# Performance work log

Hardware: AMD Instinct MI355X
Metric: run time of the kernel (lower is better)

## Reference

```python
import jax, jax.numpy as jnp
import numpy as np

NUM_HEADS = 16
EPS = 1e-6
MAX_POS = 1000

def _pos_encoding(position, d):
    pos = np.arange(position)[:, None].astype(np.float32)
    i = np.arange(d)[None, :].astype(np.float32)
    angle = pos / np.power(10000.0, 2.0 * np.floor(i / 2.0) / np.float32(d))
    angle[:, 0::2] = np.sin(angle[:, 0::2])
    angle[:, 1::2] = np.cos(angle[:, 1::2])
    return jnp.asarray(angle[None], dtype=jnp.float32)  # [1, position, d]

def _layernorm(x, g, b):
    m = x.mean(-1, keepdims=True)
    v = ((x - m) ** 2).mean(-1, keepdims=True)
    return (x - m) * jax.lax.rsqrt(v + EPS) * g + b

def setup_inputs() -> dict:
    key = jax.random.key(0)
    L, D, F, B, S = 6, 1024, 4096, 4, 512
    sd = 0.02
    ks = jax.random.split(key, 8)
    return {
        "x": jax.random.normal(ks[0], (B, S, D), jnp.float32),
        "mask": jnp.zeros((B, 1, 1, S), jnp.float32),
        "Wq": sd * jax.random.normal(ks[1], (L, D, D), jnp.float32),
        "bq": jnp.zeros((L, D), jnp.float32),
        "Wk": sd * jax.random.normal(ks[2], (L, D, D), jnp.float32),
        "bk": jnp.zeros((L, D), jnp.float32),
        "Wv": sd * jax.random.normal(ks[3], (L, D, D), jnp.float32),
        "bv": jnp.zeros((L, D), jnp.float32),
        "Wo": sd * jax.random.normal(ks[4], (L, D, D), jnp.float32),
        "bo": jnp.zeros((L, D), jnp.float32),
        "W1": sd * jax.random.normal(ks[5], (L, D, F), jnp.float32),
        "b1": jnp.zeros((L, F), jnp.float32),
        "W2": sd * jax.random.normal(ks[6], (L, F, D), jnp.float32),
        "b2": jnp.zeros((L, D), jnp.float32),
        "g1": jnp.ones((L, D), jnp.float32),
        "be1": jnp.zeros((L, D), jnp.float32),
        "g2": jnp.ones((L, D), jnp.float32),
        "be2": jnp.zeros((L, D), jnp.float32),
    }

def reference(x, mask, Wq, bq, Wk, bk, Wv, bv, Wo, bo, W1, b1, W2, b2, g1, be1, g2, be2):
    B, S, D = x.shape
    H = NUM_HEADS
    depth = D // H
    scale = 1.0 / jnp.sqrt(jnp.float32(depth))
    x = x + _pos_encoding(MAX_POS, D)[:, :S, :]

    def layer(h, p):
        (wq, bq_, wk, bk_, wv, bv_, wo, bo_, w1, b1_, w2, b2_, g1_, be1_, g2_, be2_) = p
        split = lambda t: t.reshape(B, S, H, depth).transpose(0, 2, 1, 3)
        q = split(h @ wq + bq_)
        k = split(h @ wk + bk_)
        v = split(h @ wv + bv_)
        logits = jnp.einsum('bhqd,bhkd->bhqk', q, k) * scale + mask * (-1e9)
        a = jax.nn.softmax(logits, axis=-1)
        o = jnp.einsum('bhqk,bhkd->bhqd', a, v).transpose(0, 2, 1, 3).reshape(B, S, D)
        o = o @ wo + bo_
        h1 = _layernorm(h + o, g1_, be1_)
        f = jax.nn.relu(h1 @ w1 + b1_) @ w2 + b2_
        return _layernorm(h1 + f, g2_, be2_), None

    out, _ = jax.lax.scan(layer, x, (Wq, bq, Wk, bk, Wv, bv, Wo, bo, W1, b1, W2, b2, g1, be1, g2, be2))
    return out
```

## Files before the change

kernel.cpp:

```cpp
#include <hip/hip_runtime.h>

typedef __attribute__((ext_vector_type(8))) short bf16x8;
typedef __attribute__((ext_vector_type(4))) float f32x4;
typedef unsigned short u16;

#define D_MODEL 1024
#define SEQ 512
#define BATCH 4
#define NH 16
#define FF 4096
#define NLAYER 6
#define NTOKS 2048

__device__ __forceinline__ u16 f2bf(float f) {
  unsigned int u = __float_as_uint(f);
  u += 0x7fffu + ((u >> 16) & 1u);
  return (u16)(u >> 16);
}

__device__ __forceinline__ void gload16(const void* g, void* lds) {
  __builtin_amdgcn_global_load_lds((const __attribute__((address_space(1))) void*)g,
                                   (__attribute__((address_space(3))) void*)lds, 16, 0, 0);
}

__global__ __launch_bounds__(256) void posenc_k(const float* __restrict__ x, float* __restrict__ h,
                                                u16* __restrict__ hb) {
  int row = blockIdx.x;
  int s = row & (SEQ - 1);
  int t = threadIdx.x;
  float4 v = *(const float4*)(x + (size_t)row * D_MODEL + t * 4);
  float r[4] = {v.x, v.y, v.z, v.w};
#pragma unroll
  for (int j = 0; j < 4; ++j) {
    int d = t * 4 + j;
    int p = d >> 1;
    float ang = (float)s * exp2f((float)p * (-2.0f / 1024.0f) * 13.287712379549449f);
    r[j] += (d & 1) ? cosf(ang) : sinf(ang);
  }
  float4 o = {r[0], r[1], r[2], r[3]};
  *(float4*)(h + (size_t)row * D_MODEL + t * 4) = o;
  ushort4 ob;
  ob.x = f2bf(r[0]); ob.y = f2bf(r[1]); ob.z = f2bf(r[2]); ob.w = f2bf(r[3]);
  *(ushort4*)(hb + (size_t)row * D_MODEL + t * 4) = ob;
}

#define WTP 72
__device__ __forceinline__ void wconv_body(const float* __restrict__ src, u16* __restrict__ dst,
                                           int K, int N, float scale, int nb, int kb) {
  __shared__ u16 tile[64 * WTP];
  const int t = threadIdx.x;
#pragma unroll
  for (int rr = 0; rr < 4; ++rr) {
    int k = (t >> 4) + rr * 16;
    int n4 = (t & 15) * 4;
    float4 v = *(const float4*)(src + (size_t)(kb + k) * N + nb + n4);
    tile[(n4 + 0) * WTP + k] = f2bf(v.x * scale);
    tile[(n4 + 1) * WTP + k] = f2bf(v.y * scale);
    tile[(n4 + 2) * WTP + k] = f2bf(v.z * scale);
    tile[(n4 + 3) * WTP + k] = f2bf(v.w * scale);
  }
  __syncthreads();
#pragma unroll
  for (int rr = 0; rr < 2; ++rr) {
    int n = (t >> 3) + rr * 32;
    int kq = (t & 7) * 8;
    uint4 v = *(const uint4*)&tile[n * WTP + kq];
    *(uint4*)&dst[(size_t)(nb + n) * K + kb + kq] = v;
  }
}

__global__ __launch_bounds__(256) void wconv_qkv_k(const float* __restrict__ Wq,
                                                   const float* __restrict__ Wk,
                                                   const float* __restrict__ Wv,
                                                   u16* __restrict__ dst) {
  int z = blockIdx.z, l = z / 3, which = z % 3;
  const float* src = (which == 0 ? Wq : which == 1 ? Wk : Wv) + (size_t)l * 1024 * 1024;
  u16* d = dst + (size_t)l * 3072 * 1024 + (size_t)which * 1024 * 1024;
  float scale = (which == 0) ? 0.125f : 1.0f;
  wconv_body(src, d, 1024, 1024, scale, blockIdx.x * 64, blockIdx.y * 64);
}

__global__ __launch_bounds__(256) void wconv_gen_k(const float* __restrict__ W, u16* __restrict__ dst,
                                                   int K, int N) {
  int z = blockIdx.z;
  wconv_body(W + (size_t)z * K * N, dst + (size_t)z * N * K, K, N, 1.0f,
             blockIdx.x * 64, blockIdx.y * 64);
}

__global__ __launch_bounds__(256) void bqkv_k(const float* bq, const float* bk, const float* bv,
                                              float* o) {
  int i = blockIdx.x * 256 + threadIdx.x;
  int l = i / 3072, j = i % 3072;
  float v = (j < 1024) ? bq[l * 1024 + j] * 0.125f
                       : (j < 2048 ? bk[l * 1024 + j - 1024] : bv[l * 1024 + j - 2048]);
  o[i] = v;
}

template <int OBF, int RELU, int KSPLIT>
__global__ __launch_bounds__(256) void gemm64_k(const u16* __restrict__ A, const u16* __restrict__ Bt,
                                                const float* __restrict__ bias, void* __restrict__ Cv,
                                                int N, int K) {
  __shared__ u16 As[4][64 * 32];
  __shared__ u16 Bs[4][64 * 32];
  const int t = threadIdx.x, lane = t & 63, wave = t >> 6;
  const int wm = wave >> 1, wn = wave & 1;
  const int lrow = lane & 15, lgrp = lane >> 4;
  const int m0 = blockIdx.y * 64, n0 = blockIdx.x * 64;
  const int kseg = K / KSPLIT;
  const int koff = (KSPLIT > 1) ? blockIdx.z * kseg : 0;

  f32x4 acc[2][2];
#pragma unroll
  for (int i = 0; i < 2; ++i)
#pragma unroll
    for (int j = 0; j < 2; ++j) acc[i][j] = (f32x4){0.f, 0.f, 0.f, 0.f};

  const u16* Ag = A + (size_t)m0 * K + koff;
  const u16* Bg = Bt + (size_t)n0 * K + koff;
  const int ebase = wave * 512;
  const int e = ebase + lane * 8;
  const int srow = e >> 5, skc = e & 31;

  auto stage = [&](int buf, int k0) {
    gload16(Ag + (size_t)srow * K + k0 + skc, &As[buf][ebase]);
    gload16(Bg + (size_t)srow * K + k0 + skc, &Bs[buf][ebase]);
  };

  const int nk = kseg / 32;
  stage(0, 0);
  stage(1, 32);
  stage(2, 64);
  for (int tt = 0; tt < nk; ++tt) {
    if (tt + 2 < nk) asm volatile("s_waitcnt vmcnt(4)" ::: "memory");
    else if (tt + 1 < nk) asm volatile("s_waitcnt vmcnt(2)" ::: "memory");
    else asm volatile("s_waitcnt vmcnt(0)" ::: "memory");
    __builtin_amdgcn_s_barrier();
    __builtin_amdgcn_sched_barrier(0);
    if (tt + 3 < nk) stage((tt + 3) & 3, (tt + 3) * 32);
    const int cur = tt & 3;
    bf16x8 af[2], bfr[2];
#pragma unroll
    for (int i = 0; i < 2; ++i)
      af[i] = *(const bf16x8*)&As[cur][(wm * 32 + i * 16 + lrow) * 32 + lgrp * 8];
#pragma unroll
    for (int j = 0; j < 2; ++j)
      bfr[j] = *(const bf16x8*)&Bs[cur][(wn * 32 + j * 16 + lrow) * 32 + lgrp * 8];
#pragma unroll
    for (int i = 0; i < 2; ++i)
#pragma unroll
      for (int j = 0; j < 2; ++j)
        acc[i][j] = __builtin_amdgcn_mfma_f32_16x16x32_bf16(af[i], bfr[j], acc[i][j], 0, 0, 0);
  }

  const size_t outoff = (KSPLIT > 1) ? (size_t)blockIdx.z * NTOKS * N : 0;
#pragma unroll
  for (int j = 0; j < 2; ++j) {
    int col = n0 + wn * 32 + j * 16 + lrow;
    float bv = (KSPLIT == 1 || blockIdx.z == 0) ? bias[col] : 0.f;
#pragma unroll
    for (int i = 0; i < 2; ++i) {
      int rowb = m0 + wm * 32 + i * 16 + lgrp * 4;
#pragma unroll
      for (int r = 0; r < 4; ++r) {
        float v = acc[i][j][r] + bv;
        if (RELU) v = fmaxf(v, 0.f);
        if (OBF)
          ((u16*)Cv)[(size_t)(rowb + r) * N + col] = f2bf(v);
        else
          ((float*)Cv)[outoff + (size_t)(rowb + r) * N + col] = v;
      }
    }
  }
}

__global__ __launch_bounds__(256) void vtrans_k(const u16* __restrict__ qkv, u16* __restrict__ vt) {
  __shared__ u16 tile[32][33];
  const int bx = blockIdx.x, by = blockIdx.y, b = blockIdx.z;
  const int tx = threadIdx.x & 31, ty = threadIdx.x >> 5;
#pragma unroll
  for (int i = 0; i < 32; i += 8) {
    int sidx = bx * 32 + ty + i, d = by * 32 + tx;
    tile[ty + i][tx] = qkv[(size_t)(b * SEQ + sidx) * 3072 + 2048 + d];
  }
  __syncthreads();
#pragma unroll
  for (int i = 0; i < 32; i += 8) {
    int d = by * 32 + ty + i, sidx = bx * 32 + tx;
    vt[(size_t)(b * D_MODEL + d) * SEQ + sidx] = tile[tx][ty + i];
  }
}

#define KPAD 72
__global__ __launch_bounds__(256) void attn_k(const u16* __restrict__ qkv, const u16* __restrict__ vt,
                                              const float* __restrict__ mask, u16* __restrict__ o) {
  __shared__ u16 Ks[64 * KPAD];
  __shared__ u16 Vs[64 * KPAD];
  __shared__ u16 Ps[64 * KPAD];
  const int t = threadIdx.x;
  const int lane = t & 63, wave = t >> 6;
  const int lrow = lane & 15, lgrp = lane >> 4;
  const int qb = blockIdx.x;
  const int bh = blockIdx.y;
  const int b = bh >> 4, hh = bh & 15;

  bf16x8 qf[2];
  const int qrow0 = qb * 64 + wave * 16;
#pragma unroll
  for (int kk = 0; kk < 2; ++kk)
    qf[kk] = *(const bf16x8*)(qkv + (size_t)(b * SEQ + qrow0 + lrow) * 3072 +
                              hh * 64 + kk * 32 + lgrp * 8);

  float mreg[4], lsum[4];
  f32x4 oacc[4];
#pragma unroll
  for (int r = 0; r < 4; ++r) { mreg[r] = -1e30f; lsum[r] = 0.f; }
#pragma unroll
  for (int dn = 0; dn < 4; ++dn) oacc[dn] = (f32x4){0.f, 0.f, 0.f, 0.f};

  const int sr = t >> 3, sc = t & 7;
  for (int it = 0; it < 8; ++it) {
    const int kv0 = it * 64;
#pragma unroll
    for (int half = 0; half < 2; ++half) {
      int r = sr + half * 32;
      uint4 kv4 = *(const uint4*)(qkv + (size_t)(b * SEQ + kv0 + r) * 3072 + 1024 + hh * 64 + sc * 8);
      *(uint4*)(&Ks[r * KPAD + sc * 8]) = kv4;
      uint4 vv4 = *(const uint4*)(vt + (size_t)(bh * 64 + r) * SEQ + kv0 + sc * 8);
      *(uint4*)(&Vs[r * KPAD + sc * 8]) = vv4;
    }
    __syncthreads();

    f32x4 s[4];
#pragma unroll
    for (int nt = 0; nt < 4; ++nt) s[nt] = (f32x4){0.f, 0.f, 0.f, 0.f};
#pragma unroll
    for (int nt = 0; nt < 4; ++nt)
#pragma unroll
      for (int kk = 0; kk < 2; ++kk) {
        bf16x8 kf = *(const bf16x8*)(&Ks[(nt * 16 + lrow) * KPAD + kk * 32 + lgrp * 8]);
        s[nt] = __builtin_amdgcn_mfma_f32_16x16x32_bf16(qf[kk], kf, s[nt], 0, 0, 0);
      }
    float mv[4];
#pragma unroll
    for (int nt = 0; nt < 4; ++nt) mv[nt] = mask[b * SEQ + kv0 + nt * 16 + lrow] * -1e9f;
#pragma unroll
    for (int nt = 0; nt < 4; ++nt)
#pragma unroll
      for (int r = 0; r < 4; ++r) s[nt][r] = s[nt][r] + mv[nt];

#pragma unroll
    for (int r = 0; r < 4; ++r) {
      float mx = fmaxf(fmaxf(s[0][r], s[1][r]), fmaxf(s[2][r], s[3][r]));
      mx = fmaxf(mx, __shfl_xor(mx, 1));
      mx = fmaxf(mx, __shfl_xor(mx, 2));
      mx = fmaxf(mx, __shfl_xor(mx, 4));
      mx = fmaxf(mx, __shfl_xor(mx, 8));
      float mnew = fmaxf(mreg[r], mx);
      float corr = __expf(mreg[r] - mnew);
      mreg[r] = mnew;
      float p0 = __expf(s[0][r] - mnew);
      float p1 = __expf(s[1][r] - mnew);
      float p2 = __expf(s[2][r] - mnew);
      float p3 = __expf(s[3][r] - mnew);
      float rs = p0 + p1 + p2 + p3;
      rs += __shfl_xor(rs, 1);
      rs += __shfl_xor(rs, 2);
      rs += __shfl_xor(rs, 4);
      rs += __shfl_xor(rs, 8);
      lsum[r] = lsum[r] * corr + rs;
#pragma unroll
      for (int dn = 0; dn < 4; ++dn) oacc[dn][r] = oacc[dn][r] * corr;
      int prow = wave * 16 + lgrp * 4 + r;
      Ps[prow * KPAD + 0 + lrow] = f2bf(p0);
      Ps[prow * KPAD + 16 + lrow] = f2bf(p1);
      Ps[prow * KPAD + 32 + lrow] = f2bf(p2);
      Ps[prow * KPAD + 48 + lrow] = f2bf(p3);
    }
    __syncthreads();
#pragma unroll
    for (int kk = 0; kk < 2; ++kk) {
      bf16x8 pf = *(const bf16x8*)(&Ps[(wave * 16 + lrow) * KPAD + kk * 32 + lgrp * 8]);
#pragma unroll
      for (int dn = 0; dn < 4; ++dn) {
        bf16x8 vf = *(const bf16x8*)(&Vs[(dn * 16 + lrow) * KPAD + kk * 32 + lgrp * 8]);
        oacc[dn] = __builtin_amdgcn_mfma_f32_16x16x32_bf16(pf, vf, oacc[dn], 0, 0, 0);
      }
    }
    __syncthreads();
  }
#pragma unroll
  for (int dn = 0; dn < 4; ++dn)
#pragma unroll
    for (int r = 0; r < 4; ++r) {
      int qrow = qrow0 + lgrp * 4 + r;
      o[(size_t)(b * SEQ + qrow) * D_MODEL + hh * 64 + dn * 16 + lrow] =
          f2bf(oacc[dn][r] / lsum[r]);
    }
}

__global__ __launch_bounds__(256) void ln_k(const float* __restrict__ res, const float* __restrict__ p0,
                                            const float* __restrict__ p1, const float* __restrict__ g,
                                            const float* __restrict__ be, float* __restrict__ out,
                                            u16* __restrict__ outb) {
  __shared__ float red[8];
  const int row = blockIdx.x, t = threadIdx.x;
  float4 va = *(const float4*)(res + (size_t)row * D_MODEL + t * 4);
  float4 vb = *(const float4*)(p0 + (size_t)row * D_MODEL + t * 4);
  float4 vc = *(const float4*)(p1 + (size_t)row * D_MODEL + t * 4);
  float x0 = va.x + vb.x + vc.x, x1 = va.y + vb.y + vc.y;
  float x2 = va.z + vb.z + vc.z, x3 = va.w + vb.w + vc.w;
  float s = x0 + x1 + x2 + x3;
  float s2 = x0 * x0 + x1 * x1 + x2 * x2 + x3 * x3;
#pragma unroll
  for (int off = 1; off < 64; off <<= 1) {
    s += __shfl_xor(s, off);
    s2 += __shfl_xor(s2, off);
  }
  const int wave = t >> 6, lane = t & 63;
  if (lane == 0) { red[wave] = s; red[4 + wave] = s2; }
  __syncthreads();
  s = red[0] + red[1] + red[2] + red[3];
  s2 = red[4] + red[5] + red[6] + red[7];
  float mean = s * (1.f / D_MODEL);
  float var = s2 * (1.f / D_MODEL) - mean * mean;
  float inv = rsqrtf(var + 1e-6f);
  float4 vg = *(const float4*)(g + t * 4);
  float4 ve = *(const float4*)(be + t * 4);
  float4 r;
  r.x = (x0 - mean) * inv * vg.x + ve.x;
  r.y = (x1 - mean) * inv * vg.y + ve.y;
  r.z = (x2 - mean) * inv * vg.z + ve.z;
  r.w = (x3 - mean) * inv * vg.w + ve.w;
  *(float4*)(out + (size_t)row * D_MODEL + t * 4) = r;
  if (outb) {
    ushort4 w;
    w.x = f2bf(r.x); w.y = f2bf(r.y); w.z = f2bf(r.z); w.w = f2bf(r.w);
    *(ushort4*)(outb + (size_t)row * D_MODEL + t * 4) = w;
  }
}

extern "C" void kernel_launch(void* const* d_in, const int* in_sizes, int n_in,
                              void* d_out, int out_size, void* d_ws, size_t ws_size,
                              hipStream_t stream) {
  const float* x = (const float*)d_in[0];
  const float* mask = (const float*)d_in[1];
  const float* Wq = (const float*)d_in[2];
  const float* bq = (const float*)d_in[3];
  const float* Wk = (const float*)d_in[4];
  const float* bk = (const float*)d_in[5];
  const float* Wv = (const float*)d_in[6];
  const float* bv = (const float*)d_in[7];
  const float* Wo = (const float*)d_in[8];
  const float* bo = (const float*)d_in[9];
  const float* W1 = (const float*)d_in[10];
  const float* b1 = (const float*)d_in[11];
  const float* W2 = (const float*)d_in[12];
  const float* b2 = (const float*)d_in[13];
  const float* g1 = (const float*)d_in[14];
  const float* be1 = (const float*)d_in[15];
  const float* g2 = (const float*)d_in[16];
  const float* be2 = (const float*)d_in[17];
  float* out = (float*)d_out;

  const size_t NTOK = (size_t)BATCH * SEQ;
  const size_t ACT = NTOK * D_MODEL;
  char* w = (char*)d_ws;
  float* h = (float*)w;     w += ACT * 4;
  float* h1 = (float*)w;    w += ACT * 4;
  float* op = (float*)w;    w += ACT * 4 * 2;
  u16* hb = (u16*)w;        w += ACT * 2;
  u16* h1b = (u16*)w;       w += ACT * 2;
  u16* qkvb = (u16*)w;      w += NTOK * 3072 * 2;
  u16* vt_ = (u16*)w;       w += ACT * 2;
  u16* obb = (u16*)w;       w += ACT * 2;
  u16* tb = (u16*)w;        w += NTOK * FF * 2;
  u16* wqkv_all = (u16*)w;  w += (size_t)NLAYER * 3072 * 1024 * 2;
  u16* wo_all = (u16*)w;    w += (size_t)NLAYER * 1024 * 1024 * 2;
  u16* w1_all = (u16*)w;    w += (size_t)NLAYER * 4096 * 1024 * 2;
  u16* w2_all = (u16*)w;    w += (size_t)NLAYER * 1024 * 4096 * 2;
  float* bqkv_all = (float*)w; w += (size_t)NLAYER * 3072 * 4;

  posenc_k<<<(int)NTOK, 256, 0, stream>>>(x, h, hb);
  wconv_qkv_k<<<dim3(16, 16, 18), 256, 0, stream>>>(Wq, Wk, Wv, wqkv_all);
  wconv_gen_k<<<dim3(16, 16, 6), 256, 0, stream>>>(Wo, wo_all, 1024, 1024);
  wconv_gen_k<<<dim3(64, 16, 6), 256, 0, stream>>>(W1, w1_all, 1024, 4096);
  wconv_gen_k<<<dim3(16, 64, 6), 256, 0, stream>>>(W2, w2_all, 4096, 1024);
  bqkv_k<<<72, 256, 0, stream>>>(bq, bk, bv, bqkv_all);

  for (int l = 0; l < NLAYER; ++l) {
    const u16* wqkv_t = wqkv_all + (size_t)l * 3072 * 1024;
    const u16* wo_t = wo_all + (size_t)l * 1024 * 1024;
    const u16* w1_t = w1_all + (size_t)l * 4096 * 1024;
    const u16* w2_t = w2_all + (size_t)l * 1024 * 4096;
    const float* bqkvl = bqkv_all + (size_t)l * 3072;
    const float* bol = bo + (size_t)l * D_MODEL;
    const float* b1l = b1 + (size_t)l * FF;
    const float* b2l = b2 + (size_t)l * D_MODEL;
    const float* g1l = g1 + (size_t)l * D_MODEL;
    const float* be1l = be1 + (size_t)l * D_MODEL;
    const float* g2l = g2 + (size_t)l * D_MODEL;
    const float* be2l = be2 + (size_t)l * D_MODEL;

    gemm64_k<1, 0, 1><<<dim3(48, 32), 256, 0, stream>>>(hb, wqkv_t, bqkvl, qkvb, 3072, 1024);
    vtrans_k<<<dim3(16, 32, 4), 256, 0, stream>>>(qkvb, vt_);
    attn_k<<<dim3(8, 64), 256, 0, stream>>>(qkvb, vt_, mask, obb);
    gemm64_k<0, 0, 2><<<dim3(16, 32, 2), 256, 0, stream>>>(obb, wo_t, bol, op, 1024, 1024);
    ln_k<<<(int)NTOK, 256, 0, stream>>>(h, op, op + ACT, g1l, be1l, h1, h1b);
    gemm64_k<1, 1, 1><<<dim3(64, 32), 256, 0, stream>>>(h1b, w1_t, b1l, tb, 4096, 1024);
    gemm64_k<0, 0, 2><<<dim3(16, 32, 2), 256, 0, stream>>>(tb, w2_t, b2l, op, 1024, 4096);
    ln_k<<<(int)NTOK, 256, 0, stream>>>(h1, op, op + ACT, g2l, be2l, (l == NLAYER - 1) ? out : h, hb);
  }
}
```

Measured before the change: 1.163 ms.

## Enlarge GEMM tiles to 128x128 with LDS swizzle, XCD remap and split-K 4

Replaces the 64x64 GEMM with a 128x128 tile per block. Each wave now computes a 64x64 sub-tile of 16 MFMAs per k-step, which cuts global and LDS traffic per flop. It adds an XOR swizzle on LDS columns to avoid bank conflicts, a workgroup remap so neighbouring tiles land on the same XCD, and s_setprio around MFMA bursts in the GEMM and attention kernels. Split-K for the Wo and W2 GEMMs goes from 2 to 4 to keep enough blocks, so the layernorm now sums 4 partial buffers, which adds extra fp32 traffic.

```diff
diff --git a/kernel.cpp b/kernel.cpp
--- a/kernel.cpp
+++ b/kernel.cpp
@@ -97,33 +97,49 @@
 }
 
 template <int OBF, int RELU, int KSPLIT>
-__global__ __launch_bounds__(256) void gemm64_k(const u16* __restrict__ A, const u16* __restrict__ Bt,
-                                                const float* __restrict__ bias, void* __restrict__ Cv,
-                                                int N, int K) {
-  __shared__ u16 As[4][64 * 32];
-  __shared__ u16 Bs[4][64 * 32];
+__global__ __launch_bounds__(256) void gemm128_k(const u16* __restrict__ A, const u16* __restrict__ Bt,
+                                                 const float* __restrict__ bias, void* __restrict__ Cv,
+                                                 int N, int K) {
+  __shared__ u16 As[4][128 * 32];
+  __shared__ u16 Bs[4][128 * 32];
   const int t = threadIdx.x, lane = t & 63, wave = t >> 6;
   const int wm = wave >> 1, wn = wave & 1;
   const int lrow = lane & 15, lgrp = lane >> 4;
-  const int m0 = blockIdx.y * 64, n0 = blockIdx.x * 64;
+
+  const int GX = N >> 7;
+  const int nwg = GX * 16;
+  int flat = blockIdx.y * GX + blockIdx.x;
+  int q = nwg >> 3, r = nwg & 7, xcd = flat & 7, pos = flat >> 3;
+  int logical = (xcd < r ? xcd * (q + 1) : r * (q + 1) + (xcd - r) * q) + pos;
+  const int m0 = (logical & 15) * 128, n0 = (logical >> 4) * 128;
+
   const int kseg = K / KSPLIT;
   const int koff = (KSPLIT > 1) ? blockIdx.z * kseg : 0;
 
-  f32x4 acc[2][2];
-#pragma unroll
-  for (int i = 0; i < 2; ++i)
-#pragma unroll
-    for (int j = 0; j < 2; ++j) acc[i][j] = (f32x4){0.f, 0.f, 0.f, 0.f};
+  f32x4 acc[4][4];
+#pragma unroll
+  for (int i = 0; i < 4; ++i)
+#pragma unroll
+    for (int j = 0; j < 4; ++j) acc[i][j] = (f32x4){0.f, 0.f, 0.f, 0.f};
 
   const u16* Ag = A + (size_t)m0 * K + koff;
   const u16* Bg = Bt + (size_t)n0 * K + koff;
-  const int ebase = wave * 512;
-  const int e = ebase + lane * 8;
-  const int srow = e >> 5, skc = e & 31;
 
   auto stage = [&](int buf, int k0) {
-    gload16(Ag + (size_t)srow * K + k0 + skc, &As[buf][ebase]);
-    gload16(Bg + (size_t)srow * K + k0 + skc, &Bs[buf][ebase]);
+#pragma unroll
+    for (int rr = 0; rr < 2; ++rr) {
+      int s = rr * 256 + t;
+      int row = s >> 2, cst = s & 3;
+      int csrc = cst ^ ((row >> 1) & 3);
+      gload16(Ag + (size_t)row * K + k0 + csrc * 8, &As[buf][s * 8]);
+    }
+#pragma unroll
+    for (int rr = 0; rr < 2; ++rr) {
+      int s = rr * 256 + t;
+      int row = s >> 2, cst = s & 3;
+      int csrc = cst ^ ((row >> 1) & 3);
+      gload16(Bg + (size_t)row * K + k0 + csrc * 8, &Bs[buf][s * 8]);
+    }
   };
 
   const int nk = kseg / 32;
@@ -131,35 +147,43 @@
   stage(1, 32);
   stage(2, 64);
   for (int tt = 0; tt < nk; ++tt) {
-    if (tt + 2 < nk) asm volatile("s_waitcnt vmcnt(4)" ::: "memory");
-    else if (tt + 1 < nk) asm volatile("s_waitcnt vmcnt(2)" ::: "memory");
+    if (tt + 2 < nk) asm volatile("s_waitcnt vmcnt(8)" ::: "memory");
+    else if (tt + 1 < nk) asm volatile("s_waitcnt vmcnt(4)" ::: "memory");
     else asm volatile("s_waitcnt vmcnt(0)" ::: "memory");
     __builtin_amdgcn_s_barrier();
     __builtin_amdgcn_sched_barrier(0);
     if (tt + 3 < nk) stage((tt + 3) & 3, (tt + 3) * 32);
     const int cur = tt & 3;
-    bf16x8 af[2], bfr[2];
-#pragma unroll
-    for (int i = 0; i < 2; ++i)
-      af[i] = *(const bf16x8*)&As[cur][(wm * 32 + i * 16 + lrow) * 32 + lgrp * 8];
-#pragma unroll
-    for (int j = 0; j < 2; ++j)
-      bfr[j] = *(const bf16x8*)&Bs[cur][(wn * 32 + j * 16 + lrow) * 32 + lgrp * 8];
-#pragma unroll
-    for (int i = 0; i < 2; ++i)
-#pragma unroll
-      for (int j = 0; j < 2; ++j)
+    bf16x8 af[4], bfr[4];
+#pragma unroll
+    for (int i = 0; i < 4; ++i) {
+      int row = wm * 64 + i * 16 + lrow;
+      int sl = lgrp ^ ((row >> 1) & 3);
+      af[i] = *(const bf16x8*)&As[cur][row * 32 + sl * 8];
+    }
+#pragma unroll
+    for (int j = 0; j < 4; ++j) {
+      int row = wn * 64 + j * 16 + lrow;
+      int sl = lgrp ^ ((row >> 1) & 3);
+      bfr[j] = *(const bf16x8*)&Bs[cur][row * 32 + sl * 8];
+    }
+    __builtin_amdgcn_s_setprio(1);
+#pragma unroll
+    for (int i = 0; i < 4; ++i)
+#pragma unroll
+      for (int j = 0; j < 4; ++j)
         acc[i][j] = __builtin_amdgcn_mfma_f32_16x16x32_bf16(af[i], bfr[j], acc[i][j], 0, 0, 0);
+    __builtin_amdgcn_s_setprio(0);
   }
 
   const size_t outoff = (KSPLIT > 1) ? (size_t)blockIdx.z * NTOKS * N : 0;
 #pragma unroll
-  for (int j = 0; j < 2; ++j) {
-    int col = n0 + wn * 32 + j * 16 + lrow;
+  for (int j = 0; j < 4; ++j) {
+    int col = n0 + wn * 64 + j * 16 + lrow;
     float bv = (KSPLIT == 1 || blockIdx.z == 0) ? bias[col] : 0.f;
 #pragma unroll
-    for (int i = 0; i < 2; ++i) {
-      int rowb = m0 + wm * 32 + i * 16 + lgrp * 4;
+    for (int i = 0; i < 4; ++i) {
+      int rowb = m0 + wm * 64 + i * 16 + lgrp * 4;
 #pragma unroll
       for (int r = 0; r < 4; ++r) {
         float v = acc[i][j][r] + bv;
@@ -233,6 +257,7 @@
     f32x4 s[4];
 #pragma unroll
     for (int nt = 0; nt < 4; ++nt) s[nt] = (f32x4){0.f, 0.f, 0.f, 0.f};
+    __builtin_amdgcn_s_setprio(1);
 #pragma unroll
     for (int nt = 0; nt < 4; ++nt)
 #pragma unroll
@@ -240,6 +265,7 @@
         bf16x8 kf = *(const bf16x8*)(&Ks[(nt * 16 + lrow) * KPAD + kk * 32 + lgrp * 8]);
         s[nt] = __builtin_amdgcn_mfma_f32_16x16x32_bf16(qf[kk], kf, s[nt], 0, 0, 0);
       }
+    __builtin_amdgcn_s_setprio(0);
     float mv[4];
 #pragma unroll
     for (int nt = 0; nt < 4; ++nt) mv[nt] = mask[b * SEQ + kv0 + nt * 16 + lrow] * -1e9f;
@@ -277,6 +303,7 @@
       Ps[prow * KPAD + 48 + lrow] = f2bf(p3);
     }
     __syncthreads();
+    __builtin_amdgcn_s_setprio(1);
 #pragma unroll
     for (int kk = 0; kk < 2; ++kk) {
       bf16x8 pf = *(const bf16x8*)(&Ps[(wave * 16 + lrow) * KPAD + kk * 32 + lgrp * 8]);
@@ -286,6 +313,7 @@
         oacc[dn] = __builtin_amdgcn_mfma_f32_16x16x32_bf16(pf, vf, oacc[dn], 0, 0, 0);
       }
     }
+    __builtin_amdgcn_s_setprio(0);
     __syncthreads();
   }
 #pragma unroll
@@ -298,17 +326,19 @@
     }
 }
 
-__global__ __launch_bounds__(256) void ln_k(const float* __restrict__ res, const float* __restrict__ p0,
-                                            const float* __restrict__ p1, const float* __restrict__ g,
-                                            const float* __restrict__ be, float* __restrict__ out,
-                                            u16* __restrict__ outb) {
+template <int P>
+__global__ __launch_bounds__(256) void ln_k(const float* __restrict__ res, const float* __restrict__ parts,
+                                            const float* __restrict__ g, const float* __restrict__ be,
+                                            float* __restrict__ out, u16* __restrict__ outb) {
   __shared__ float red[8];
   const int row = blockIdx.x, t = threadIdx.x;
   float4 va = *(const float4*)(res + (size_t)row * D_MODEL + t * 4);
-  float4 vb = *(const float4*)(p0 + (size_t)row * D_MODEL + t * 4);
-  float4 vc = *(const float4*)(p1 + (size_t)row * D_MODEL + t * 4);
-  float x0 = va.x + vb.x + vc.x, x1 = va.y + vb.y + vc.y;
-  float x2 = va.z + vb.z + vc.z, x3 = va.w + vb.w + vc.w;
+  float x0 = va.x, x1 = va.y, x2 = va.z, x3 = va.w;
+#pragma unroll
+  for (int p = 0; p < P; ++p) {
+    float4 vp = *(const float4*)(parts + (size_t)p * NTOKS * D_MODEL + (size_t)row * D_MODEL + t * 4);
+    x0 += vp.x; x1 += vp.y; x2 += vp.z; x3 += vp.w;
+  }
   float s = x0 + x1 + x2 + x3;
   float s2 = x0 * x0 + x1 * x1 + x2 * x2 + x3 * x3;
 #pragma unroll
@@ -367,7 +397,7 @@
   char* w = (char*)d_ws;
   float* h = (float*)w;     w += ACT * 4;
   float* h1 = (float*)w;    w += ACT * 4;
-  float* op = (float*)w;    w += ACT * 4 * 2;
+  float* op = (float*)w;    w += ACT * 4 * 4;
   u16* hb = (u16*)w;        w += ACT * 2;
   u16* h1b = (u16*)w;       w += ACT * 2;
   u16* qkvb = (u16*)w;      w += NTOK * 3072 * 2;
@@ -401,13 +431,13 @@
     const float* g2l = g2 + (size_t)l * D_MODEL;
     const float* be2l = be2 + (size_t)l * D_MODEL;
 
-    gemm64_k<1, 0, 1><<<dim3(48, 32), 256, 0, stream>>>(hb, wqkv_t, bqkvl, qkvb, 3072, 1024);
+    gemm128_k<1, 0, 1><<<dim3(24, 16), 256, 0, stream>>>(hb, wqkv_t, bqkvl, qkvb, 3072, 1024);
     vtrans_k<<<dim3(16, 32, 4), 256, 0, stream>>>(qkvb, vt_);
     attn_k<<<dim3(8, 64), 256, 0, stream>>>(qkvb, vt_, mask, obb);
-    gemm64_k<0, 0, 2><<<dim3(16, 32, 2), 256, 0, stream>>>(obb, wo_t, bol, op, 1024, 1024);
-    ln_k<<<(int)NTOK, 256, 0, stream>>>(h, op, op + ACT, g1l, be1l, h1, h1b);
-    gemm64_k<1, 1, 1><<<dim3(64, 32), 256, 0, stream>>>(h1b, w1_t, b1l, tb, 4096, 1024);
-    gemm64_k<0, 0, 2><<<dim3(16, 32, 2), 256, 0, stream>>>(tb, w2_t, b2l, op, 1024, 4096);
-    ln_k<<<(int)NTOK, 256, 0, stream>>>(h1, op, op + ACT, g2l, be2l, (l == NLAYER - 1) ? out : h, hb);
-  }
-}
+    gemm128_k<0, 0, 4><<<dim3(8, 16, 4), 256, 0, stream>>>(obb, wo_t, bol, op, 1024, 1024);
+    ln_k<4><<<(int)NTOK, 256, 0, stream>>>(h, op, g1l, be1l, h1, h1b);
+    gemm128_k<1, 1, 1><<<dim3(32, 16), 256, 0, stream>>>(h1b, w1_t, b1l, tb, 4096, 1024);
+    gemm128_k<0, 0, 4><<<dim3(8, 16, 4), 256, 0, stream>>>(tb, w2_t, b2l, op, 1024, 4096);
+    ln_k<4><<<(int)NTOK, 256, 0, stream>>>(h1, op, g2l, be2l, (l == NLAYER - 1) ? out : h, hb);
+  }
+}
```

Measured after the change: 1.039 ms. 1.12x faster.
